# Optimization experiments

Measured on AMD Instinct MI355X. Metric: run time of the kernel, lower is better.

Reference implementation:

```python
import jax, jax.numpy as jnp
import numpy as np

B, T, E, A = 8, 2048, 1024, 1024


def setup_inputs() -> dict:
    key = jax.random.key(0)
    k1, k2, k3, k4 = jax.random.split(key, 4)
    embedded = jax.random.normal(k1, (B, T, E), dtype=jnp.float32)
    s = 1.0 / np.sqrt(E)
    # nn.Linear(E, A, bias=False) stores weight of shape (A, E); y = x @ W^T
    Wq = jax.random.uniform(k2, (A, E), dtype=jnp.float32, minval=-s, maxval=s)
    Wk = jax.random.uniform(k3, (A, E), dtype=jnp.float32, minval=-s, maxval=s)
    Wv = jax.random.uniform(k4, (A, E), dtype=jnp.float32, minval=-s, maxval=s)
    return {"embedded": embedded, "Wq": Wq, "Wk": Wk, "Wv": Wv}


def reference(embedded, Wq, Wk, Wv):
    # q, k, v: [B, T, A]
    q = jnp.einsum("bte,ae->bta", embedded, Wq)
    k = jnp.einsum("bte,ae->bta", embedded, Wk)
    v = jnp.einsum("bte,ae->bta", embedded, Wv)
    scale = 1.0 / jnp.sqrt(jnp.asarray(Wq.shape[0], dtype=q.dtype))
    # causal scores: [B, T, T]
    scores = jnp.einsum("bqa,bka->bqk", q, k) * scale
    t = scores.shape[-1]
    causal = jnp.tril(jnp.ones((t, t), dtype=bool))
    scores = jnp.where(causal, scores, jnp.asarray(-jnp.inf, dtype=scores.dtype))
    attn = jax.nn.softmax(scores, axis=-1)
    return jnp.einsum("bqk,bka->bqa", attn, v)
```

## Files before the change

kernel.cpp:

```cpp
#include <hip/hip_runtime.h>
#include <hip/hip_bf16.h>
#include <stdint.h>


#define BB 8
#define TT 2048
#define EE 1024
#define AA 1024
#define MM (BB * TT)

typedef short bf16x8 __attribute__((ext_vector_type(8)));
typedef float f32x4 __attribute__((ext_vector_type(4)));

#define GLOAD_LDS16(g, l)                                                      \
  __builtin_amdgcn_global_load_lds(                                            \
      (const __attribute__((address_space(1))) void*)(g),                      \
      (__attribute__((address_space(3))) void*)(l), 16, 0, 0)

#define SBAR()                               \
  do {                                       \
    __builtin_amdgcn_sched_barrier(0);       \
    __builtin_amdgcn_s_barrier();            \
    __builtin_amdgcn_sched_barrier(0);       \
  } while (0)

#define LGKM0()                                          \
  do {                                                   \
    asm volatile("s_waitcnt lgkmcnt(0)" ::: "memory");   \
    __builtin_amdgcn_sched_barrier(0);                   \
  } while (0)

#define VMCNT(n)                                              \
  do {                                                        \
    asm volatile("s_waitcnt vmcnt(" #n ")" ::: "memory");     \
    __builtin_amdgcn_sched_barrier(0);                        \
  } while (0)

__device__ __forceinline__ void gemm256_core(
    const short* __restrict__ gA, int lda, int a0row,
    const short* __restrict__ gB, int ldb, int b0row, int NT, short* As,
    short* Bs, f32x4 (*acc)[4]) {
  const int tid = threadIdx.x;
  const int lane = tid & 63;
  const int w = tid >> 6;
  const int wr = w >> 2, wc = w & 3;
  const int lrow = lane & 15;
  const int lk8 = (lane >> 4) * 8;
  const int swz = ((lrow >> 3) & 1) << 4;
  const int baseA = (((wr * 128 + lrow) * 32) + lk8) ^ swz;
  const int baseB = (((wc * 64 + lrow) * 32) + lk8) ^ swz;

  const short* pA[2];
  const short* pB[2];
#pragma unroll
  for (int i = 0; i < 2; ++i) {
    int chunk = 2 * w + i;
    int P = chunk * 1024 + lane * 16;
    int L = P ^ (((P >> 9) & 1) << 5);
    int row = L >> 6;
    int kb2 = (L & 63) >> 1;
    pA[i] = gA + (size_t)(a0row + row) * lda + kb2;
    pB[i] = gB + (size_t)(b0row + row) * ldb + kb2;
  }

#pragma unroll
  for (int tl = 0; tl < 2; ++tl) {
    short* Ac = As + tl * 16384;
    short* Bc = Bs + tl * 16384;
#pragma unroll
    for (int s = 0; s < 2; ++s) {
      int off = tl * 64 + s * 32;
      GLOAD_LDS16(pA[0] + off, Ac + s * 8192 + (2 * w) * 512 + lane * 8);
      GLOAD_LDS16(pA[1] + off, Ac + s * 8192 + (2 * w + 1) * 512 + lane * 8);
      GLOAD_LDS16(pB[0] + off, Bc + s * 8192 + (2 * w) * 512 + lane * 8);
      GLOAD_LDS16(pB[1] + off, Bc + s * 8192 + (2 * w + 1) * 512 + lane * 8);
    }
  }
  VMCNT(8);
  SBAR();

  for (int t = 0; t < NT; ++t) {
    short* Ac = As + (t & 1) * 16384;
    short* Bc = Bs + (t & 1) * 16384;
    const bool stg = (t < NT - 2);
    const int off2 = (t + 2) * 64;
    bf16x8 a0[4], a1[4], a2[4], a3[4], b0[4], b1[4];

#pragma unroll
    for (int m = 0; m < 4; ++m) a0[m] = *(const bf16x8*)&Ac[baseA + m * 512];
#pragma unroll
    for (int n = 0; n < 4; ++n) b0[n] = *(const bf16x8*)&Bc[baseB + n * 512];
    SBAR();
    LGKM0();
    __builtin_amdgcn_s_setprio(1);
#pragma unroll
    for (int m = 0; m < 4; ++m)
#pragma unroll
      for (int n = 0; n < 4; ++n)
        acc[m][n] = __builtin_amdgcn_mfma_f32_16x16x32_bf16(a0[m], b0[n],
                                                            acc[m][n], 0, 0, 0);
    __builtin_amdgcn_s_setprio(0);
    SBAR();

#pragma unroll
    for (int m = 0; m < 4; ++m)
      a1[m] = *(const bf16x8*)&Ac[baseA + (m + 4) * 512];
#pragma unroll
    for (int m = 0; m < 4; ++m)
      a2[m] = *(const bf16x8*)&Ac[8192 + baseA + m * 512];
    if (stg) {
      GLOAD_LDS16(pB[0] + off2, Bc + (2 * w) * 512 + lane * 8);
      GLOAD_LDS16(pB[1] + off2, Bc + (2 * w + 1) * 512 + lane * 8);
    }
    SBAR();
    LGKM0();
    __builtin_amdgcn_s_setprio(1);
#pragma unroll
    for (int m = 0; m < 4; ++m)
#pragma unroll
      for (int n = 0; n < 4; ++n)
        acc[m + 4][n] = __builtin_amdgcn_mfma_f32_16x16x32_bf16(
            a1[m], b0[n], acc[m + 4][n], 0, 0, 0);
    __builtin_amdgcn_s_setprio(0);
    SBAR();

#pragma unroll
    for (int m = 0; m < 4; ++m)
      a3[m] = *(const bf16x8*)&Ac[8192 + baseA + (m + 4) * 512];
#pragma unroll
    for (int n = 0; n < 4; ++n)
      b1[n] = *(const bf16x8*)&Bc[8192 + baseB + n * 512];
    if (stg) {
      GLOAD_LDS16(pA[0] + off2, Ac + (2 * w) * 512 + lane * 8);
      GLOAD_LDS16(pA[1] + off2, Ac + (2 * w + 1) * 512 + lane * 8);
    }
    SBAR();
    LGKM0();
    __builtin_amdgcn_s_setprio(1);
#pragma unroll
    for (int m = 0; m < 4; ++m)
#pragma unroll
      for (int n = 0; n < 4; ++n)
        acc[m][n] = __builtin_amdgcn_mfma_f32_16x16x32_bf16(a2[m], b1[n],
                                                            acc[m][n], 0, 0, 0);
    __builtin_amdgcn_s_setprio(0);
    SBAR();

    if (stg) {
      GLOAD_LDS16(pA[0] + off2 + 32, Ac + 8192 + (2 * w) * 512 + lane * 8);
      GLOAD_LDS16(pA[1] + off2 + 32, Ac + 8192 + (2 * w + 1) * 512 + lane * 8);
      GLOAD_LDS16(pB[0] + off2 + 32, Bc + 8192 + (2 * w) * 512 + lane * 8);
      GLOAD_LDS16(pB[1] + off2 + 32, Bc + 8192 + (2 * w + 1) * 512 + lane * 8);
    }
    if (t < NT - 1) {
      if (stg) {
        VMCNT(8);
      } else {
        VMCNT(0);
      }
    }
    SBAR();
    __builtin_amdgcn_s_setprio(1);
#pragma unroll
    for (int m = 0; m < 4; ++m)
#pragma unroll
      for (int n = 0; n < 4; ++n)
        acc[m + 4][n] = __builtin_amdgcn_mfma_f32_16x16x32_bf16(
            a3[m], b1[n], acc[m + 4][n], 0, 0, 0);
    __builtin_amdgcn_s_setprio(0);
    SBAR();
  }
}

__global__ __launch_bounds__(512, 2) void qkv_gemm8(
    const short* __restrict__ xb, const short* __restrict__ Wb,
    short* __restrict__ qkv) {
  __shared__ __align__(16) short As[32768];
  __shared__ __align__(16) short Bs[32768];
  int f = blockIdx.x;
  int s = (f & 7) * 96 + (f >> 3);
  int mt = s / 12, nt = s % 12;
  int z = nt >> 2, ntl = nt & 3;
  const short* gB = Wb + (size_t)z * AA * EE + (size_t)(ntl * 256) * EE;
  f32x4 acc[8][4];
#pragma unroll
  for (int m = 0; m < 8; ++m)
#pragma unroll
    for (int n = 0; n < 4; ++n) acc[m][n] = (f32x4){0.f, 0.f, 0.f, 0.f};
  gemm256_core(xb, EE, mt * 256, gB, EE, 0, EE / 64, As, Bs, acc);

  short* o = qkv + (size_t)z * MM * AA;
  int lane = threadIdx.x & 63, w = threadIdx.x >> 6, wr = w >> 2, wc = w & 3;
  int lrow = lane & 15, lk4 = (lane >> 4) * 4;
  int row0 = mt * 256 + wr * 128;
  int col0 = ntl * 256 + wc * 64;
#pragma unroll
  for (int m = 0; m < 8; ++m)
#pragma unroll
    for (int n = 0; n < 4; ++n)
#pragma unroll
      for (int r = 0; r < 4; ++r) {
        int row = row0 + m * 16 + lk4 + r;
        int col = col0 + n * 16 + lrow;
        __hip_bfloat16 h = __float2bfloat16(acc[m][n][r]);
        o[(size_t)row * AA + col] = *(short*)&h;
      }
}

__device__ __forceinline__ void stage_tile(const short* __restrict__ g,
                                           size_t stride, short* lds, int tid) {
#pragma unroll
  for (int r = 0; r < 4; ++r) {
    int t = r * 256 + tid;
    int row = t >> 3;
    int c = (t & 7) * 8;
    GLOAD_LDS16(g + (size_t)row * stride + c, lds + (size_t)t * 8);
  }
}

__device__ __forceinline__ void mfma_step(const short* As, const short* Bs,
                                          f32x4 acc[4][4], int lane, int wr,
                                          int wc) {
  int lrow = lane & 15;
  int lk = (lane >> 4) * 8;
#pragma unroll
  for (int kk = 0; kk < 64; kk += 32) {
    bf16x8 a[4], b[4];
#pragma unroll
    for (int i = 0; i < 4; ++i)
      a[i] = *(const bf16x8*)&As[(wr * 64 + i * 16 + lrow) * 64 + kk + lk];
#pragma unroll
    for (int j = 0; j < 4; ++j)
      b[j] = *(const bf16x8*)&Bs[(wc * 64 + j * 16 + lrow) * 64 + kk + lk];
#pragma unroll
    for (int i = 0; i < 4; ++i)
#pragma unroll
      for (int j = 0; j < 4; ++j)
        acc[i][j] =
            __builtin_amdgcn_mfma_f32_16x16x32_bf16(a[i], b[j], acc[i][j], 0, 0, 0);
  }
}

__global__ void cvt_bf16(const float* __restrict__ src, short* __restrict__ dst,
                         int n4) {
  int stride = gridDim.x * blockDim.x;
  for (int i = blockIdx.x * blockDim.x + threadIdx.x; i < n4; i += stride) {
    float4 v = ((const float4*)src)[i];
    __hip_bfloat16 h0 = __float2bfloat16(v.x);
    __hip_bfloat16 h1 = __float2bfloat16(v.y);
    __hip_bfloat16 h2 = __float2bfloat16(v.z);
    __hip_bfloat16 h3 = __float2bfloat16(v.w);
    short4 o;
    o.x = *(short*)&h0;
    o.y = *(short*)&h1;
    o.z = *(short*)&h2;
    o.w = *(short*)&h3;
    ((short4*)dst)[i] = o;
  }
}

__global__ void cvt_w3(const float* __restrict__ wq, const float* __restrict__ wk,
                       const float* __restrict__ wv, short* __restrict__ dst) {
  const int n4 = AA * EE / 4;
  int stride = gridDim.x * blockDim.x;
  for (int i = blockIdx.x * blockDim.x + threadIdx.x; i < 3 * n4; i += stride) {
    const float* src = (i < n4) ? wq : (i < 2 * n4 ? wk : wv);
    int ii = (i < n4) ? i : (i < 2 * n4 ? i - n4 : i - 2 * n4);
    float4 v = ((const float4*)src)[ii];
    __hip_bfloat16 h0 = __float2bfloat16(v.x);
    __hip_bfloat16 h1 = __float2bfloat16(v.y);
    __hip_bfloat16 h2 = __float2bfloat16(v.z);
    __hip_bfloat16 h3 = __float2bfloat16(v.w);
    short4 o;
    o.x = *(short*)&h0;
    o.y = *(short*)&h1;
    o.z = *(short*)&h2;
    o.w = *(short*)&h3;
    ((short4*)dst)[i] = o;
  }
}

__global__ __launch_bounds__(256) void transpose_v(const short* __restrict__ Vb,
                                                   short* __restrict__ Vt) {
  __shared__ __align__(16) short lds[64 * 72];
  int t0 = blockIdx.x * 64;
  int d0 = blockIdx.y * 64;
  int b = blockIdx.z;
  int tid = threadIdx.x;
  const short* src = Vb + ((size_t)b * TT + t0) * AA + d0;
#pragma unroll
  for (int r = 0; r < 2; ++r) {
    int t = r * 256 + tid;
    int row = t >> 3;
    int c = (t & 7) * 8;
    *(bf16x8*)&lds[row * 72 + c] = *(const bf16x8*)&src[(size_t)row * AA + c];
  }
  __syncthreads();
  short* dst = Vt + ((size_t)b * AA + d0) * TT + t0;
#pragma unroll
  for (int r = 0; r < 2; ++r) {
    int t = r * 256 + tid;
    int d = t >> 3;
    int c = (t & 7) * 8;
    bf16x8 w;
#pragma unroll
    for (int e = 0; e < 8; ++e) w[e] = lds[(c + e) * 72 + d];
    *(bf16x8*)&dst[(size_t)d * TT + c] = w;
  }
}

__global__ __launch_bounds__(256) void score_gemm(const short* __restrict__ Qb,
                                                  const short* __restrict__ Kb,
                                                  short* __restrict__ Pu,
                                                  float* __restrict__ lsum) {
  int f = blockIdx.x;
  int b = f & 7;
  int j = f >> 3;
  int mt = 0;
  while ((mt + 1) * (mt + 2) / 2 <= j) ++mt;
  int nt = j - mt * (mt + 1) / 2;
  int q0 = mt * 128, c0 = nt * 128;

  __shared__ __align__(16) short As[128 * 64];
  __shared__ __align__(16) short Bs[128 * 64];
  int tid = threadIdx.x;
  int lane = tid & 63, wid = tid >> 6, wr = wid >> 1, wc = wid & 1;
  const short* Q = Qb + (size_t)b * TT * AA;
  const short* K = Kb + (size_t)b * TT * AA;
  f32x4 acc[4][4];
#pragma unroll
  for (int i = 0; i < 4; ++i)
#pragma unroll
    for (int jj = 0; jj < 4; ++jj) acc[i][jj] = (f32x4){0.f, 0.f, 0.f, 0.f};

  for (int k0 = 0; k0 < AA; k0 += 64) {
    stage_tile(Q + (size_t)q0 * AA + k0, AA, As, tid);
    stage_tile(K + (size_t)c0 * AA + k0, AA, Bs, tid);
    __syncthreads();
    mfma_step(As, Bs, acc, lane, wr, wc);
    __syncthreads();
  }
  const float scale = 0.03125f;
  short* P = Pu + (size_t)b * TT * TT;
  int lrow = lane & 15, lk4 = (lane >> 4) * 4;
#pragma unroll
  for (int i = 0; i < 4; ++i) {
#pragma unroll
    for (int r = 0; r < 4; ++r) {
      int q = q0 + wr * 64 + i * 16 + lk4 + r;
      float rs = 0.f;
#pragma unroll
      for (int jj = 0; jj < 4; ++jj) {
        int kx = c0 + wc * 64 + jj * 16 + lrow;
        float e = (kx <= q) ? __expf(acc[i][jj][r] * scale) : 0.f;
        rs += e;
        __hip_bfloat16 h = __float2bfloat16(e);
        P[(size_t)q * TT + kx] = *(short*)&h;
      }
      rs += __shfl_xor(rs, 1);
      rs += __shfl_xor(rs, 2);
      rs += __shfl_xor(rs, 4);
      rs += __shfl_xor(rs, 8);
      if (lrow == 0) atomicAdd(&lsum[b * TT + q], rs);
    }
  }
}

__global__ __launch_bounds__(256) void pv_gemm(const short* __restrict__ Pu,
                                               const short* __restrict__ Vt,
                                               const float* __restrict__ lsum,
                                               float* __restrict__ out) {
  int f = blockIdx.x;
  int b = f & 7;
  int j = f >> 3;
  int p = j >> 3;
  int nt = j & 7;
  int n0 = nt * 128;

  __shared__ __align__(16) short As[128 * 64];
  __shared__ __align__(16) short Bs[128 * 64];
  int tid = threadIdx.x;
  int lane = tid & 63, wid = tid >> 6, wr = wid >> 1, wc = wid & 1;
  const short* P = Pu + (size_t)b * TT * TT;
  const short* V = Vt + (size_t)b * AA * TT;
  int lrow = lane & 15, lk4 = (lane >> 4) * 4;

#pragma unroll
  for (int s = 0; s < 2; ++s) {
    int mt = s ? (15 - p) : p;
    int q0 = mt * 128;
    f32x4 acc[4][4];
#pragma unroll
    for (int i = 0; i < 4; ++i)
#pragma unroll
      for (int jj = 0; jj < 4; ++jj) acc[i][jj] = (f32x4){0.f, 0.f, 0.f, 0.f};

    int kend = q0 + 128;
    for (int k0 = 0; k0 < kend; k0 += 64) {
      stage_tile(P + (size_t)q0 * TT + k0, TT, As, tid);
      stage_tile(V + (size_t)n0 * TT + k0, TT, Bs, tid);
      __syncthreads();
      mfma_step(As, Bs, acc, lane, wr, wc);
      __syncthreads();
    }
#pragma unroll
    for (int i = 0; i < 4; ++i) {
#pragma unroll
      for (int r = 0; r < 4; ++r) {
        int q = q0 + wr * 64 + i * 16 + lk4 + r;
        float linv = 1.0f / lsum[b * TT + q];
#pragma unroll
        for (int jj = 0; jj < 4; ++jj) {
          int d = n0 + wc * 64 + jj * 16 + lrow;
          out[((size_t)(b * TT + q)) * AA + d] = acc[i][jj][r] * linv;
        }
      }
    }
  }
}

extern "C" void kernel_launch(void* const* d_in, const int* in_sizes, int n_in,
                              void* d_out, int out_size, void* d_ws,
                              size_t ws_size, hipStream_t stream) {
  const float* x = (const float*)d_in[0];
  const float* Wq = (const float*)d_in[1];
  const float* Wk = (const float*)d_in[2];
  const float* Wv = (const float*)d_in[3];

  char* ws = (char*)d_ws;
  size_t oWb = 0;
  size_t oQb = oWb + (size_t)3 * AA * EE * 2;
  size_t oKb = oQb + (size_t)MM * AA * 2;
  size_t oVb = oKb + (size_t)MM * AA * 2;
  size_t oVt = oVb + (size_t)MM * AA * 2;
  size_t oLs = oVt + (size_t)MM * AA * 2;
  size_t oXb = oLs + (size_t)MM * 4;
  size_t oPu = oXb;

  short* Wb = (short*)(ws + oWb);
  short* Qb = (short*)(ws + oQb);
  short* Kb = (short*)(ws + oKb);
  short* Vb = (short*)(ws + oVb);
  short* Vt = (short*)(ws + oVt);
  float* Ls = (float*)(ws + oLs);
  short* Xb = (short*)(ws + oXb);
  short* Pu = (short*)(ws + oPu);

  cvt_bf16<<<2048, 256, 0, stream>>>(x, Xb, MM * EE / 4);
  cvt_w3<<<768, 256, 0, stream>>>(Wq, Wk, Wv, Wb);
  hipMemsetAsync(Ls, 0, (size_t)MM * 4, stream);

  qkv_gemm8<<<768, 512, 0, stream>>>(Xb, Wb, Qb);
  transpose_v<<<dim3(32, 16, 8), 256, 0, stream>>>(Vb, Vt);
  score_gemm<<<1088, 256, 0, stream>>>(Qb, Kb, Pu, Ls);
  pv_gemm<<<512, 256, 0, stream>>>(Pu, Vt, Ls, (float*)d_out);
}
```

Measured before the change: 293.7 us.

## Software-pipeline LDS fragment loads across MFMA phases in QKV GEMM core

Restructures the 256x256 GEMM main loop so LDS fragment reads for the next phase are issued before the current MFMA block. Partial lgkmcnt waits replace full drains, and the next tile's a0/b0 fragments are prefetched at the end of each iteration. Global-to-LDS staging is reordered into finer A/B half-chunks with adjusted vmcnt thresholds. The aim is to hide LDS latency behind matrix math, at the cost of more live registers and fragile waitcnt accounting.

```diff
diff --git a/kernel.cpp b/kernel.cpp
--- a/kernel.cpp
+++ b/kernel.cpp
@@ -24,10 +24,10 @@
     __builtin_amdgcn_sched_barrier(0);       \
   } while (0)
 
-#define LGKM0()                                          \
-  do {                                                   \
-    asm volatile("s_waitcnt lgkmcnt(0)" ::: "memory");   \
-    __builtin_amdgcn_sched_barrier(0);                   \
+#define LGKM(n)                                               \
+  do {                                                        \
+    asm volatile("s_waitcnt lgkmcnt(" #n ")" ::: "memory");   \
+    __builtin_amdgcn_sched_barrier(0);                        \
   } while (0)
 
 #define VMCNT(n)                                              \
@@ -35,6 +35,8 @@
     asm volatile("s_waitcnt vmcnt(" #n ")" ::: "memory");     \
     __builtin_amdgcn_sched_barrier(0);                        \
   } while (0)
+
+#define MFMA16(a, b, c) __builtin_amdgcn_mfma_f32_16x16x32_bf16((a), (b), (c), 0, 0, 0)
 
 __device__ __forceinline__ void gemm256_core(
     const short* __restrict__ gA, int lda, int a0row,
@@ -43,10 +45,10 @@
   const int tid = threadIdx.x;
   const int lane = tid & 63;
   const int w = tid >> 6;
-  const int wr = w >> 2, wc = w & 3;
   const int lrow = lane & 15;
   const int lk8 = (lane >> 4) * 8;
   const int swz = ((lrow >> 3) & 1) << 4;
+  const int wr = w >> 2, wc = w & 3;
   const int baseA = (((wr * 128 + lrow) * 32) + lk8) ^ swz;
   const int baseB = (((wc * 64 + lrow) * 32) + lk8) ^ swz;
 
@@ -63,113 +65,120 @@
     pB[i] = gB + (size_t)(b0row + row) * ldb + kb2;
   }
 
-#pragma unroll
-  for (int tl = 0; tl < 2; ++tl) {
-    short* Ac = As + tl * 16384;
-    short* Bc = Bs + tl * 16384;
-#pragma unroll
-    for (int s = 0; s < 2; ++s) {
-      int off = tl * 64 + s * 32;
-      GLOAD_LDS16(pA[0] + off, Ac + s * 8192 + (2 * w) * 512 + lane * 8);
-      GLOAD_LDS16(pA[1] + off, Ac + s * 8192 + (2 * w + 1) * 512 + lane * 8);
-      GLOAD_LDS16(pB[0] + off, Bc + s * 8192 + (2 * w) * 512 + lane * 8);
-      GLOAD_LDS16(pB[1] + off, Bc + s * 8192 + (2 * w + 1) * 512 + lane * 8);
-    }
-  }
-  VMCNT(8);
+#define STG_A(tl, s)                                                           \
+  do {                                                                         \
+    int _o = (tl) * 64 + (s) * 32;                                             \
+    short* _d = As + (((tl) & 1) << 14) + ((s) << 13);                         \
+    GLOAD_LDS16(pA[0] + _o, _d + (2 * w) * 512 + lane * 8);                    \
+    GLOAD_LDS16(pA[1] + _o, _d + (2 * w + 1) * 512 + lane * 8);                \
+  } while (0)
+#define STG_B(tl, s)                                                           \
+  do {                                                                         \
+    int _o = (tl) * 64 + (s) * 32;                                             \
+    short* _d = Bs + (((tl) & 1) << 14) + ((s) << 13);                         \
+    GLOAD_LDS16(pB[0] + _o, _d + (2 * w) * 512 + lane * 8);                    \
+    GLOAD_LDS16(pB[1] + _o, _d + (2 * w + 1) * 512 + lane * 8);                \
+  } while (0)
+
+  STG_B(0, 0); STG_A(0, 0); STG_B(0, 1); STG_A(0, 1);
+  bf16x8 a0[4], b0[4];
+  if (NT > 1) {
+    STG_B(1, 0); STG_A(1, 0); STG_B(1, 1);
+    VMCNT(6);
+  } else {
+    VMCNT(0);
+  }
   SBAR();
+#pragma unroll
+  for (int m = 0; m < 4; ++m) a0[m] = *(const bf16x8*)&As[baseA + m * 512];
+#pragma unroll
+  for (int n = 0; n < 4; ++n) b0[n] = *(const bf16x8*)&Bs[baseB + n * 512];
 
   for (int t = 0; t < NT; ++t) {
-    short* Ac = As + (t & 1) * 16384;
-    short* Bc = Bs + (t & 1) * 16384;
-    const bool stg = (t < NT - 2);
-    const int off2 = (t + 2) * 64;
-    bf16x8 a0[4], a1[4], a2[4], a3[4], b0[4], b1[4];
-
-#pragma unroll
-    for (int m = 0; m < 4; ++m) a0[m] = *(const bf16x8*)&Ac[baseA + m * 512];
-#pragma unroll
-    for (int n = 0; n < 4; ++n) b0[n] = *(const bf16x8*)&Bc[baseB + n * 512];
-    SBAR();
-    LGKM0();
+    const short* Ac = As + ((t & 1) << 14);
+    const short* Bc = Bs + ((t & 1) << 14);
+    const short* An = As + (((t + 1) & 1) << 14);
+    const short* Bn = Bs + (((t + 1) & 1) << 14);
+    bf16x8 a1[4], a2[4], a3[4], b1[4];
+
+    if (t < NT - 1) {
+      STG_A(t + 1, 1);
+      VMCNT(8);
+    } else {
+      VMCNT(0);
+    }
+    SBAR();
+#pragma unroll
+    for (int m = 0; m < 4; ++m)
+      a1[m] = *(const bf16x8*)&Ac[baseA + (m + 4) * 512];
+#pragma unroll
+    for (int m = 0; m < 4; ++m)
+      a2[m] = *(const bf16x8*)&Ac[8192 + baseA + m * 512];
+    LGKM(8);
     __builtin_amdgcn_s_setprio(1);
 #pragma unroll
     for (int m = 0; m < 4; ++m)
 #pragma unroll
-      for (int n = 0; n < 4; ++n)
-        acc[m][n] = __builtin_amdgcn_mfma_f32_16x16x32_bf16(a0[m], b0[n],
-                                                            acc[m][n], 0, 0, 0);
+      for (int n = 0; n < 4; ++n) acc[m][n] = MFMA16(a0[m], b0[n], acc[m][n]);
     __builtin_amdgcn_s_setprio(0);
     SBAR();
 
-#pragma unroll
-    for (int m = 0; m < 4; ++m)
-      a1[m] = *(const bf16x8*)&Ac[baseA + (m + 4) * 512];
-#pragma unroll
-    for (int m = 0; m < 4; ++m)
-      a2[m] = *(const bf16x8*)&Ac[8192 + baseA + m * 512];
-    if (stg) {
-      GLOAD_LDS16(pB[0] + off2, Bc + (2 * w) * 512 + lane * 8);
-      GLOAD_LDS16(pB[1] + off2, Bc + (2 * w + 1) * 512 + lane * 8);
-    }
-    SBAR();
-    LGKM0();
-    __builtin_amdgcn_s_setprio(1);
-#pragma unroll
-    for (int m = 0; m < 4; ++m)
-#pragma unroll
-      for (int n = 0; n < 4; ++n)
-        acc[m + 4][n] = __builtin_amdgcn_mfma_f32_16x16x32_bf16(
-            a1[m], b0[n], acc[m + 4][n], 0, 0, 0);
-    __builtin_amdgcn_s_setprio(0);
-    SBAR();
-
-#pragma unroll
-    for (int m = 0; m < 4; ++m)
-      a3[m] = *(const bf16x8*)&Ac[8192 + baseA + (m + 4) * 512];
+    if (t < NT - 2) STG_B(t + 2, 0);
+    SBAR();
 #pragma unroll
     for (int n = 0; n < 4; ++n)
       b1[n] = *(const bf16x8*)&Bc[8192 + baseB + n * 512];
-    if (stg) {
-      GLOAD_LDS16(pA[0] + off2, Ac + (2 * w) * 512 + lane * 8);
-      GLOAD_LDS16(pA[1] + off2, Ac + (2 * w + 1) * 512 + lane * 8);
-    }
-    SBAR();
-    LGKM0();
+    LGKM(4);
     __builtin_amdgcn_s_setprio(1);
 #pragma unroll
     for (int m = 0; m < 4; ++m)
 #pragma unroll
       for (int n = 0; n < 4; ++n)
-        acc[m][n] = __builtin_amdgcn_mfma_f32_16x16x32_bf16(a2[m], b1[n],
-                                                            acc[m][n], 0, 0, 0);
+        acc[m + 4][n] = MFMA16(a1[m], b0[n], acc[m + 4][n]);
     __builtin_amdgcn_s_setprio(0);
     SBAR();
 
-    if (stg) {
-      GLOAD_LDS16(pA[0] + off2 + 32, Ac + 8192 + (2 * w) * 512 + lane * 8);
-      GLOAD_LDS16(pA[1] + off2 + 32, Ac + 8192 + (2 * w + 1) * 512 + lane * 8);
-      GLOAD_LDS16(pB[0] + off2 + 32, Bc + 8192 + (2 * w) * 512 + lane * 8);
-      GLOAD_LDS16(pB[1] + off2 + 32, Bc + 8192 + (2 * w + 1) * 512 + lane * 8);
-    }
+    if (t < NT - 2) STG_A(t + 2, 0);
+    SBAR();
+#pragma unroll
+    for (int m = 0; m < 4; ++m)
+      a3[m] = *(const bf16x8*)&Ac[8192 + baseA + (m + 4) * 512];
+    LGKM(4);
+    __builtin_amdgcn_s_setprio(1);
+#pragma unroll
+    for (int m = 0; m < 4; ++m)
+#pragma unroll
+      for (int n = 0; n < 4; ++n) acc[m][n] = MFMA16(a2[m], b1[n], acc[m][n]);
+    __builtin_amdgcn_s_setprio(0);
+    SBAR();
+
+    if (t < NT - 2) {
+      STG_B(t + 2, 1);
+      VMCNT(10);
+    } else if (t == NT - 2) {
+      VMCNT(4);
+    }
+    SBAR();
     if (t < NT - 1) {
-      if (stg) {
-        VMCNT(8);
-      } else {
-        VMCNT(0);
-      }
-    }
-    SBAR();
+#pragma unroll
+      for (int m = 0; m < 4; ++m) a0[m] = *(const bf16x8*)&An[baseA + m * 512];
+#pragma unroll
+      for (int n = 0; n < 4; ++n) b0[n] = *(const bf16x8*)&Bn[baseB + n * 512];
+      LGKM(8);
+    } else {
+      LGKM(0);
+    }
     __builtin_amdgcn_s_setprio(1);
 #pragma unroll
     for (int m = 0; m < 4; ++m)
 #pragma unroll
       for (int n = 0; n < 4; ++n)
-        acc[m + 4][n] = __builtin_amdgcn_mfma_f32_16x16x32_bf16(
-            a3[m], b1[n], acc[m + 4][n], 0, 0, 0);
+        acc[m + 4][n] = MFMA16(a3[m], b1[n], acc[m + 4][n]);
     __builtin_amdgcn_s_setprio(0);
     SBAR();
   }
+#undef STG_A
+#undef STG_B
 }
 
 __global__ __launch_bounds__(512, 2) void qkv_gemm8(
@@ -302,10 +311,10 @@
     int t = r * 256 + tid;
     int d = t >> 3;
     int c = (t & 7) * 8;
-    bf16x8 w;
-#pragma unroll
-    for (int e = 0; e < 8; ++e) w[e] = lds[(c + e) * 72 + d];
-    *(bf16x8*)&dst[(size_t)d * TT + c] = w;
+    bf16x8 wv;
+#pragma unroll
+    for (int e = 0; e < 8; ++e) wv[e] = lds[(c + e) * 72 + d];
+    *(bf16x8*)&dst[(size_t)d * TT + c] = wv;
   }
 }
 
```

New measurement: 305.5 us. 1.04x slower.

## Fuse V transpose into QKV GEMM epilogue and memset into weight convert

Applied to the files above, without the earlier changes.

The QKV GEMM now writes the V tile transposed straight to Vt: it stages the tile in XOR-swizzled shared memory and emits 16-byte row stores, which removes the separate transpose_v kernel and the Vb buffer round trip. The lsum zeroing moves from hipMemsetAsync into cvt_w3, which drops one launch. The cost is two extra block barriers and an LDS staging pass in the V blocks of the GEMM, plus reuse of the GEMM's LDS for the epilogue.

```diff
diff --git a/kernel.cpp b/kernel.cpp
--- a/kernel.cpp
+++ b/kernel.cpp
@@ -174,9 +174,10 @@
 
 __global__ __launch_bounds__(512, 2) void qkv_gemm8(
     const short* __restrict__ xb, const short* __restrict__ Wb,
-    short* __restrict__ qkv) {
-  __shared__ __align__(16) short As[32768];
-  __shared__ __align__(16) short Bs[32768];
+    short* __restrict__ qk, short* __restrict__ Vt) {
+  __shared__ __align__(16) short SH[65536];
+  short* As = SH;
+  short* Bs = SH + 32768;
   int f = blockIdx.x;
   int s = (f & 7) * 96 + (f >> 3);
   int mt = s / 12, nt = s % 12;
@@ -189,22 +190,57 @@
     for (int n = 0; n < 4; ++n) acc[m][n] = (f32x4){0.f, 0.f, 0.f, 0.f};
   gemm256_core(xb, EE, mt * 256, gB, EE, 0, EE / 64, As, Bs, acc);
 
-  short* o = qkv + (size_t)z * MM * AA;
-  int lane = threadIdx.x & 63, w = threadIdx.x >> 6, wr = w >> 2, wc = w & 3;
+  int tid = threadIdx.x;
+  int lane = tid & 63, w = tid >> 6, wr = w >> 2, wc = w & 3;
   int lrow = lane & 15, lk4 = (lane >> 4) * 4;
-  int row0 = mt * 256 + wr * 128;
-  int col0 = ntl * 256 + wc * 64;
-#pragma unroll
-  for (int m = 0; m < 8; ++m)
-#pragma unroll
-    for (int n = 0; n < 4; ++n)
-#pragma unroll
-      for (int r = 0; r < 4; ++r) {
-        int row = row0 + m * 16 + lk4 + r;
-        int col = col0 + n * 16 + lrow;
-        __hip_bfloat16 h = __float2bfloat16(acc[m][n][r]);
-        o[(size_t)row * AA + col] = *(short*)&h;
+
+  if (z < 2) {
+    short* o = qk + (size_t)z * MM * AA;
+    int row0 = mt * 256 + wr * 128;
+    int col0 = ntl * 256 + wc * 64;
+#pragma unroll
+    for (int m = 0; m < 8; ++m)
+#pragma unroll
+      for (int n = 0; n < 4; ++n)
+#pragma unroll
+        for (int r = 0; r < 4; ++r) {
+          int row = row0 + m * 16 + lk4 + r;
+          int col = col0 + n * 16 + lrow;
+          __hip_bfloat16 h = __float2bfloat16(acc[m][n][r]);
+          o[(size_t)row * AA + col] = *(short*)&h;
+        }
+  } else {
+    __syncthreads();
+    int lr0 = wr * 128, lc0 = wc * 64;
+#pragma unroll
+    for (int m = 0; m < 8; ++m)
+#pragma unroll
+      for (int n = 0; n < 4; ++n)
+#pragma unroll
+        for (int r = 0; r < 4; ++r) {
+          int lr = lr0 + m * 16 + lk4 + r;
+          int lc = lc0 + n * 16 + lrow;
+          __hip_bfloat16 h = __float2bfloat16(acc[m][n][r]);
+          SH[lc * 256 + (lr ^ ((lc & 7) << 3))] = *(short*)&h;
+        }
+    __syncthreads();
+    int row0 = mt * 256;
+    int bq = row0 >> 11;
+    int t0 = row0 & 2047;
+#pragma unroll
+    for (int pass = 0; pass < 4; ++pass) {
+      int lc = pass * 64 + (tid >> 3);
+      int d = ntl * 256 + lc;
+      size_t dst = ((size_t)bq * AA + d) * TT + t0;
+      int sw = (lc & 7) << 3;
+#pragma unroll
+      for (int g = 0; g < 4; ++g) {
+        int lr = (tid & 7) * 8 + g * 64;
+        bf16x8 vv = *(const bf16x8*)&SH[lc * 256 + (lr ^ sw)];
+        *(bf16x8*)&Vt[dst + lr] = vv;
       }
+    }
+  }
 }
 
 __device__ __forceinline__ void stage_tile(const short* __restrict__ g,
@@ -260,10 +296,13 @@
 }
 
 __global__ void cvt_w3(const float* __restrict__ wq, const float* __restrict__ wk,
-                       const float* __restrict__ wv, short* __restrict__ dst) {
+                       const float* __restrict__ wv, short* __restrict__ dst,
+                       float* __restrict__ Ls) {
   const int n4 = AA * EE / 4;
+  int gid = blockIdx.x * blockDim.x + threadIdx.x;
+  if (gid < MM) Ls[gid] = 0.f;
   int stride = gridDim.x * blockDim.x;
-  for (int i = blockIdx.x * blockDim.x + threadIdx.x; i < 3 * n4; i += stride) {
+  for (int i = gid; i < 3 * n4; i += stride) {
     const float* src = (i < n4) ? wq : (i < 2 * n4 ? wk : wv);
     int ii = (i < n4) ? i : (i < 2 * n4 ? i - n4 : i - 2 * n4);
     float4 v = ((const float4*)src)[ii];
@@ -280,35 +319,6 @@
   }
 }
 
-__global__ __launch_bounds__(256) void transpose_v(const short* __restrict__ Vb,
-                                                   short* __restrict__ Vt) {
-  __shared__ __align__(16) short lds[64 * 72];
-  int t0 = blockIdx.x * 64;
-  int d0 = blockIdx.y * 64;
-  int b = blockIdx.z;
-  int tid = threadIdx.x;
-  const short* src = Vb + ((size_t)b * TT + t0) * AA + d0;
-#pragma unroll
-  for (int r = 0; r < 2; ++r) {
-    int t = r * 256 + tid;
-    int row = t >> 3;
-    int c = (t & 7) * 8;
-    *(bf16x8*)&lds[row * 72 + c] = *(const bf16x8*)&src[(size_t)row * AA + c];
-  }
-  __syncthreads();
-  short* dst = Vt + ((size_t)b * AA + d0) * TT + t0;
-#pragma unroll
-  for (int r = 0; r < 2; ++r) {
-    int t = r * 256 + tid;
-    int d = t >> 3;
-    int c = (t & 7) * 8;
-    bf16x8 w;
-#pragma unroll
-    for (int e = 0; e < 8; ++e) w[e] = lds[(c + e) * 72 + d];
-    *(bf16x8*)&dst[(size_t)d * TT + c] = w;
-  }
-}
-
 __global__ __launch_bounds__(256) void score_gemm(const short* __restrict__ Qb,
                                                   const short* __restrict__ Kb,
                                                   short* __restrict__ Pu,
@@ -431,8 +441,7 @@
   size_t oWb = 0;
   size_t oQb = oWb + (size_t)3 * AA * EE * 2;
   size_t oKb = oQb + (size_t)MM * AA * 2;
-  size_t oVb = oKb + (size_t)MM * AA * 2;
-  size_t oVt = oVb + (size_t)MM * AA * 2;
+  size_t oVt = oKb + (size_t)MM * AA * 2;
   size_t oLs = oVt + (size_t)MM * AA * 2;
   size_t oXb = oLs + (size_t)MM * 4;
   size_t oPu = oXb;
@@ -440,18 +449,15 @@
   short* Wb = (short*)(ws + oWb);
   short* Qb = (short*)(ws + oQb);
   short* Kb = (short*)(ws + oKb);
-  short* Vb = (short*)(ws + oVb);
   short* Vt = (short*)(ws + oVt);
   float* Ls = (float*)(ws + oLs);
   short* Xb = (short*)(ws + oXb);
   short* Pu = (short*)(ws + oPu);
 
   cvt_bf16<<<2048, 256, 0, stream>>>(x, Xb, MM * EE / 4);
-  cvt_w3<<<768, 256, 0, stream>>>(Wq, Wk, Wv, Wb);
-  hipMemsetAsync(Ls, 0, (size_t)MM * 4, stream);
-
-  qkv_gemm8<<<768, 512, 0, stream>>>(Xb, Wb, Qb);
-  transpose_v<<<dim3(32, 16, 8), 256, 0, stream>>>(Vb, Vt);
+  cvt_w3<<<768, 256, 0, stream>>>(Wq, Wk, Wv, Wb, Ls);
+
+  qkv_gemm8<<<768, 512, 0, stream>>>(Xb, Wb, Qb, Vt);
   score_gemm<<<1088, 256, 0, stream>>>(Qb, Kb, Pu, Ls);
   pv_gemm<<<512, 256, 0, stream>>>(Pu, Vt, Ls, (float*)d_out);
 }
```

Result: faster. 265.7 us (-9.5%).
